# Performance work log

Hardware: AMD Instinct MI355X
Metric: run time of the kernel (lower is better)

## Reference

```python
import jax, jax.numpy as jnp
import numpy as np

TAU = 1.0
TOP_K = 2
TOP_C = 8
EPS = 1e-12


def _stable_softmax(v):
    # matches torch: exp(v - max) / (sum + 1e-12)
    e = jnp.exp(v - jnp.max(v, axis=-1, keepdims=True))
    return e / (jnp.sum(e, axis=-1, keepdims=True) + EPS)


def setup_inputs() -> dict:
    key = jax.random.key(0)
    kx, kw = jax.random.split(key)
    B, D, M = 16384, 2048, 64
    x = jax.random.normal(kx, (B, D), dtype=jnp.float32)
    W = jax.random.normal(kw, (M, D), dtype=jnp.float32) * (1.0 / np.sqrt(D))
    return {"x": x, "W": W}


def reference(x, W):
    # router GEMM: [B, D] x [M, D]^T -> [B, M]
    router_logits = jnp.einsum('bd,md->bm', x, W)
    scaled_logits = router_logits / TAU
    probs = _stable_softmax(scaled_logits)
    # double top-k: first candidates (top_c), then top_k among candidates
    topc_vals, topc_idx = jax.lax.top_k(scaled_logits, TOP_C)   # [B, C]
    topk_vals, topk_pos_in_C = jax.lax.top_k(topc_vals, TOP_K)  # [B, K]
    topk_idx = jnp.take_along_axis(topc_idx, topk_pos_in_C, axis=1)
    topk_weights = _stable_softmax(topk_vals)
    return (topk_idx.astype(jnp.int64), topk_weights, probs, topc_idx.astype(jnp.int64))
```

## Files before the change

### kernel.cpp

```cpp
#include <hip/hip_runtime.h>


typedef __attribute__((ext_vector_type(8))) short short8;
typedef __attribute__((ext_vector_type(4))) float f32x4;

constexpr int Bq = 16384;
constexpr int Dk = 2048;
constexpr int Me = 64;
constexpr int WAVES = 8;
constexpr int ROWS = 32;
constexpr int KCHUNK = Dk / WAVES;
constexpr int NT = KCHUNK / 32;

constexpr size_t OFF_TOPK_IDX = 0;
constexpr size_t OFF_TOPK_W   = (size_t)Bq * 2;
constexpr size_t OFF_PROBS    = (size_t)Bq * 4;
constexpr size_t OFF_TOPC_IDX = (size_t)Bq * 4 + (size_t)Bq * 64;

__device__ __forceinline__ unsigned f2bf2(float lo, float hi) {
  unsigned r;
  asm("v_cvt_pk_bf16_f32 %0, %1, %2" : "=v"(r) : "v"(lo), "v"(hi));
  return r;
}
__device__ __forceinline__ float bflo(unsigned u) { return __builtin_bit_cast(float, u << 16); }
__device__ __forceinline__ float bfhi(unsigned u) { return __builtin_bit_cast(float, u & 0xFFFF0000u); }

__device__ __forceinline__ void split3(const float af[8], short8& s0, short8& s1, short8& s2) {
  uint4 q0, q1, q2;
  unsigned* p0 = &q0.x; unsigned* p1 = &q1.x; unsigned* p2 = &q2.x;
  #pragma unroll
  for (int p = 0; p < 4; ++p) {
    float a = af[2 * p], b = af[2 * p + 1];
    unsigned c0 = f2bf2(a, b);
    float r0a = a - bflo(c0), r0b = b - bfhi(c0);
    unsigned c1 = f2bf2(r0a, r0b);
    float r1a = r0a - bflo(c1), r1b = r0b - bfhi(c1);
    unsigned c2 = f2bf2(r1a, r1b);
    p0[p] = c0; p1[p] = c1; p2[p] = c2;
  }
  s0 = __builtin_bit_cast(short8, q0);
  s1 = __builtin_bit_cast(short8, q1);
  s2 = __builtin_bit_cast(short8, q2);
}

__global__ void wsplit_kernel(const float* __restrict__ W,
                              unsigned short* __restrict__ w0,
                              unsigned short* __restrict__ w1,
                              unsigned short* __restrict__ w2) {
  int t = blockIdx.x * blockDim.x + threadIdx.x;
  int kt = t >> 8, n = (t >> 6) & 3, L = t & 63;
  int e  = n * 16 + (L & 15);
  int kb = kt * 32 + ((L >> 4) << 3);
  const float* src = W + (size_t)e * Dk + kb;
  float4 a = *reinterpret_cast<const float4*>(src);
  float4 b = *reinterpret_cast<const float4*>(src + 4);
  float af[8] = {a.x, a.y, a.z, a.w, b.x, b.y, b.z, b.w};
  short8 s0, s1, s2;
  split3(af, s0, s1, s2);
  *reinterpret_cast<short8*>(w0 + (size_t)t * 8) = s0;
  *reinterpret_cast<short8*>(w1 + (size_t)t * 8) = s1;
  *reinterpret_cast<short8*>(w2 + (size_t)t * 8) = s2;
}

__global__ __launch_bounds__(512, 2)
void gating_mfma(const float* __restrict__ x,
                 const unsigned short* __restrict__ w0,
                 const unsigned short* __restrict__ w1,
                 const unsigned short* __restrict__ w2,
                 float* __restrict__ out) {
  __shared__ __align__(16) char smem[WAVES * ROWS * 36 * 4];
  typedef float XaT[ROWS][36];
  XaT* xa = reinterpret_cast<XaT*>(smem);
  typedef float PartT[ROWS][68];
  PartT* part = reinterpret_cast<PartT*>(smem);

  const int tid  = threadIdx.x;
  const int wv   = tid >> 6;
  const int L    = tid & 63;
  const int lidx = L & 15;
  const int kgrp = L >> 4;
  const int rowBase = blockIdx.x * ROWS;
  const int kBase = wv * KCHUNK;

  const int srow = L >> 3;
  const int sc4  = (L & 7) << 2;
  const float* xg0 = x + (size_t)(rowBase +      srow) * Dk + kBase + sc4;
  const float* xg1 = x + (size_t)(rowBase +  8 + srow) * Dk + kBase + sc4;
  const float* xg2 = x + (size_t)(rowBase + 16 + srow) * Dk + kBase + sc4;
  const float* xg3 = x + (size_t)(rowBase + 24 + srow) * Dk + kBase + sc4;

  const size_t bbase = (size_t)kBase * 64 + (size_t)L * 8;

  f32x4 acc[2][4];
  #pragma unroll
  for (int rg = 0; rg < 2; ++rg)
    #pragma unroll
    for (int n = 0; n < 4; ++n) acc[rg][n] = (f32x4){0.f, 0.f, 0.f, 0.f};

  *reinterpret_cast<float4*>(&xa[wv][     srow][sc4]) = *reinterpret_cast<const float4*>(xg0);
  *reinterpret_cast<float4*>(&xa[wv][ 8 + srow][sc4]) = *reinterpret_cast<const float4*>(xg1);
  *reinterpret_cast<float4*>(&xa[wv][16 + srow][sc4]) = *reinterpret_cast<const float4*>(xg2);
  *reinterpret_cast<float4*>(&xa[wv][24 + srow][sc4]) = *reinterpret_cast<const float4*>(xg3);

  #pragma unroll 1
  for (int kt = 0; kt < NT; ++kt) {
    float4 aLo0 = *reinterpret_cast<const float4*>(&xa[wv][     lidx][kgrp * 8]);
    float4 aHi0 = *reinterpret_cast<const float4*>(&xa[wv][     lidx][kgrp * 8 + 4]);
    float4 aLo1 = *reinterpret_cast<const float4*>(&xa[wv][16 + lidx][kgrp * 8]);
    float4 aHi1 = *reinterpret_cast<const float4*>(&xa[wv][16 + lidx][kgrp * 8 + 4]);

    float4 h0, h1, h2, h3;
    if (kt < NT - 1) {
      h0 = *reinterpret_cast<const float4*>(xg0 + (kt + 1) * 32);
      h1 = *reinterpret_cast<const float4*>(xg1 + (kt + 1) * 32);
      h2 = *reinterpret_cast<const float4*>(xg2 + (kt + 1) * 32);
      h3 = *reinterpret_cast<const float4*>(xg3 + (kt + 1) * 32);
    }

    const size_t to = bbase + (size_t)kt * 2048;

    short8 b0[4];
    #pragma unroll
    for (int n = 0; n < 4; ++n) b0[n] = *reinterpret_cast<const short8*>(w0 + to + n * 512);

    float af0[8] = {aLo0.x, aLo0.y, aLo0.z, aLo0.w, aHi0.x, aHi0.y, aHi0.z, aHi0.w};
    float af1[8] = {aLo1.x, aLo1.y, aLo1.z, aLo1.w, aHi1.x, aHi1.y, aHi1.z, aHi1.w};
    short8 xs00, xs10, xs20, xs01, xs11, xs21;
    split3(af0, xs00, xs10, xs20);
    split3(af1, xs01, xs11, xs21);

    short8 b1[4];
    #pragma unroll
    for (int n = 0; n < 4; ++n) b1[n] = *reinterpret_cast<const short8*>(w1 + to + n * 512);

    #pragma unroll
    for (int n = 0; n < 4; ++n) acc[0][n] = __builtin_amdgcn_mfma_f32_16x16x32_bf16(xs00, b0[n], acc[0][n], 0, 0, 0);
    #pragma unroll
    for (int n = 0; n < 4; ++n) acc[1][n] = __builtin_amdgcn_mfma_f32_16x16x32_bf16(xs01, b0[n], acc[1][n], 0, 0, 0);
    #pragma unroll
    for (int n = 0; n < 4; ++n) acc[0][n] = __builtin_amdgcn_mfma_f32_16x16x32_bf16(xs10, b0[n], acc[0][n], 0, 0, 0);
    #pragma unroll
    for (int n = 0; n < 4; ++n) acc[1][n] = __builtin_amdgcn_mfma_f32_16x16x32_bf16(xs11, b0[n], acc[1][n], 0, 0, 0);
    #pragma unroll
    for (int n = 0; n < 4; ++n) acc[0][n] = __builtin_amdgcn_mfma_f32_16x16x32_bf16(xs20, b0[n], acc[0][n], 0, 0, 0);
    #pragma unroll
    for (int n = 0; n < 4; ++n) acc[1][n] = __builtin_amdgcn_mfma_f32_16x16x32_bf16(xs21, b0[n], acc[1][n], 0, 0, 0);

    short8 b2[4];
    #pragma unroll
    for (int n = 0; n < 4; ++n) b2[n] = *reinterpret_cast<const short8*>(w2 + to + n * 512);

    #pragma unroll
    for (int n = 0; n < 4; ++n) acc[0][n] = __builtin_amdgcn_mfma_f32_16x16x32_bf16(xs00, b1[n], acc[0][n], 0, 0, 0);
    #pragma unroll
    for (int n = 0; n < 4; ++n) acc[1][n] = __builtin_amdgcn_mfma_f32_16x16x32_bf16(xs01, b1[n], acc[1][n], 0, 0, 0);
    #pragma unroll
    for (int n = 0; n < 4; ++n) acc[0][n] = __builtin_amdgcn_mfma_f32_16x16x32_bf16(xs10, b1[n], acc[0][n], 0, 0, 0);
    #pragma unroll
    for (int n = 0; n < 4; ++n) acc[1][n] = __builtin_amdgcn_mfma_f32_16x16x32_bf16(xs11, b1[n], acc[1][n], 0, 0, 0);

    #pragma unroll
    for (int n = 0; n < 4; ++n) acc[0][n] = __builtin_amdgcn_mfma_f32_16x16x32_bf16(xs00, b2[n], acc[0][n], 0, 0, 0);
    #pragma unroll
    for (int n = 0; n < 4; ++n) acc[1][n] = __builtin_amdgcn_mfma_f32_16x16x32_bf16(xs01, b2[n], acc[1][n], 0, 0, 0);

    if (kt < NT - 1) {
      *reinterpret_cast<float4*>(&xa[wv][     srow][sc4]) = h0;
      *reinterpret_cast<float4*>(&xa[wv][ 8 + srow][sc4]) = h1;
      *reinterpret_cast<float4*>(&xa[wv][16 + srow][sc4]) = h2;
      *reinterpret_cast<float4*>(&xa[wv][24 + srow][sc4]) = h3;
    }
  }

  __syncthreads();
  if (wv >= 4) {
    #pragma unroll
    for (int rg = 0; rg < 2; ++rg)
      #pragma unroll
      for (int n = 0; n < 4; ++n)
        #pragma unroll
        for (int r = 0; r < 4; ++r)
          part[wv - 4][rg * 16 + kgrp * 4 + r][n * 16 + lidx] = acc[rg][n][r];
  }
  __syncthreads();
  if (wv < 4) {
    #pragma unroll
    for (int rg = 0; rg < 2; ++rg)
      #pragma unroll
      for (int n = 0; n < 4; ++n)
        #pragma unroll
        for (int r = 0; r < 4; ++r) {
          float s = acc[rg][n][r] + part[wv][rg * 16 + kgrp * 4 + r][n * 16 + lidx];
          part[wv][rg * 16 + kgrp * 4 + r][n * 16 + lidx] = s;
        }
  }
  __syncthreads();

  const int row = tid >> 4;
  const int g   = tid & 15;
  const int c4  = g * 4;
  const size_t grow = (size_t)rowBase + row;

  float4 v = {0.f, 0.f, 0.f, 0.f};
  #pragma unroll
  for (int p = 0; p < 4; ++p) {
    float4 t = *reinterpret_cast<const float4*>(&part[p][row][c4]);
    v.x += t.x; v.y += t.y; v.z += t.z; v.w += t.w;
  }
  float pv[4] = {v.x, v.y, v.z, v.w};

  float mx = fmaxf(fmaxf(pv[0], pv[1]), fmaxf(pv[2], pv[3]));
  #pragma unroll
  for (int m = 1; m < 16; m <<= 1) mx = fmaxf(mx, __shfl_xor(mx, m));
  float e[4], sum = 0.f;
  #pragma unroll
  for (int j = 0; j < 4; ++j) { e[j] = expf(pv[j] - mx); sum += e[j]; }
  #pragma unroll
  for (int m = 1; m < 16; m <<= 1) sum += __shfl_xor(sum, m);
  const float inv = 1.f / (sum + 1e-12f);
  float4 pw = {e[0] * inv, e[1] * inv, e[2] * inv, e[3] * inv};
  *reinterpret_cast<float4*>(out + OFF_PROBS + grow * 64 + c4) = pw;

  unsigned taken = 0;
  int bidx0 = 0, bidx1 = 0;
  float tv0 = 0.f, tv1 = 0.f;
  #pragma unroll 1
  for (int rank = 0; rank < 8; ++rank) {
    float best = -3.4e38f;
    int bl = -1;
    #pragma unroll
    for (int j = 0; j < 4; ++j)
      if (!((taken >> j) & 1u) && pv[j] > best) { best = pv[j]; bl = j; }
    int bidx = (bl >= 0) ? (c4 + bl) : (1 << 30);
    #pragma unroll
    for (int m = 1; m < 16; m <<= 1) {
      float ov = __shfl_xor(best, m);
      int   oi = __shfl_xor(bidx, m);
      if (ov > best || (ov == best && oi < bidx)) { best = ov; bidx = oi; }
    }
    if (bidx >= c4 && bidx < c4 + 4) taken |= 1u << (bidx - c4);
    if (g == 0) out[OFF_TOPC_IDX + grow * 8 + rank] = (float)bidx;
    if (rank == 0) { tv0 = best; bidx0 = bidx; }
    if (rank == 1) { tv1 = best; bidx1 = bidx; }
  }

  if (g == 0) {
    out[OFF_TOPK_IDX + grow * 2 + 0] = (float)bidx0;
    out[OFF_TOPK_IDX + grow * 2 + 1] = (float)bidx1;
    const float e1  = expf(tv1 - tv0);
    const float den = 1.f + e1 + 1e-12f;
    out[OFF_TOPK_W + grow * 2 + 0] = 1.f / den;
    out[OFF_TOPK_W + grow * 2 + 1] = e1 / den;
  }
}

extern "C" void kernel_launch(void* const* d_in, const int* in_sizes, int n_in,
                              void* d_out, int out_size, void* d_ws, size_t ws_size,
                              hipStream_t stream) {
  const float* x = (const float*)d_in[0];
  const float* W = (const float*)d_in[1];
  float* out = (float*)d_out;

  unsigned short* w0 = (unsigned short*)d_ws;
  unsigned short* w1 = w0 + (size_t)Me * Dk;
  unsigned short* w2 = w1 + (size_t)Me * Dk;

  hipLaunchKernelGGL(wsplit_kernel, dim3((Me * Dk / 8) / 256), dim3(256), 0, stream, W, w0, w1, w2);
  hipLaunchKernelGGL(gating_mfma, dim3(Bq / ROWS), dim3(512), 0, stream, x, w0, w1, w2, out);
}
```

Measured before the change: 46.08 us.

## Double row tile to 64 per block to improve weight reuse

Each block now handles 64 rows instead of 32, so every wave loads its W fragments once for four 16-row groups. This halves the weight traffic per row and adds more MFMA work per load. The epilogue is reorganized so 8 threads each cover 8 experts of a row. The cost is more registers and shared memory, launch bounds that drop to one block per SM, and half as many blocks (256), which may leave some of the MI355X's CUs idle.

```diff
diff --git a/kernel.cpp b/kernel.cpp
--- a/kernel.cpp
+++ b/kernel.cpp
@@ -8,9 +8,10 @@
 constexpr int Dk = 2048;
 constexpr int Me = 64;
 constexpr int WAVES = 8;
-constexpr int ROWS = 32;
+constexpr int ROWS = 64;
 constexpr int KCHUNK = Dk / WAVES;
 constexpr int NT = KCHUNK / 32;
+constexpr int XLD = 34;
 
 constexpr size_t OFF_TOPK_IDX = 0;
 constexpr size_t OFF_TOPK_W   = (size_t)Bq * 2;
@@ -62,14 +63,14 @@
   *reinterpret_cast<short8*>(w2 + (size_t)t * 8) = s2;
 }
 
-__global__ __launch_bounds__(512, 2)
+__global__ __launch_bounds__(512, 1)
 void gating_mfma(const float* __restrict__ x,
                  const unsigned short* __restrict__ w0,
                  const unsigned short* __restrict__ w1,
                  const unsigned short* __restrict__ w2,
                  float* __restrict__ out) {
-  __shared__ __align__(16) char smem[WAVES * ROWS * 36 * 4];
-  typedef float XaT[ROWS][36];
+  __shared__ __align__(16) char smem[WAVES * ROWS * XLD * 4];
+  typedef float XaT[ROWS][XLD];
   XaT* xa = reinterpret_cast<XaT*>(smem);
   typedef float PartT[ROWS][68];
   PartT* part = reinterpret_cast<PartT*>(smem);
@@ -84,37 +85,35 @@
 
   const int srow = L >> 3;
   const int sc4  = (L & 7) << 2;
-  const float* xg0 = x + (size_t)(rowBase +      srow) * Dk + kBase + sc4;
-  const float* xg1 = x + (size_t)(rowBase +  8 + srow) * Dk + kBase + sc4;
-  const float* xg2 = x + (size_t)(rowBase + 16 + srow) * Dk + kBase + sc4;
-  const float* xg3 = x + (size_t)(rowBase + 24 + srow) * Dk + kBase + sc4;
+  const float* xgb = x + (size_t)(rowBase + srow) * Dk + kBase + sc4;
 
   const size_t bbase = (size_t)kBase * 64 + (size_t)L * 8;
 
-  f32x4 acc[2][4];
-  #pragma unroll
-  for (int rg = 0; rg < 2; ++rg)
+  f32x4 acc[4][4];
+  #pragma unroll
+  for (int rg = 0; rg < 4; ++rg)
     #pragma unroll
     for (int n = 0; n < 4; ++n) acc[rg][n] = (f32x4){0.f, 0.f, 0.f, 0.f};
 
-  *reinterpret_cast<float4*>(&xa[wv][     srow][sc4]) = *reinterpret_cast<const float4*>(xg0);
-  *reinterpret_cast<float4*>(&xa[wv][ 8 + srow][sc4]) = *reinterpret_cast<const float4*>(xg1);
-  *reinterpret_cast<float4*>(&xa[wv][16 + srow][sc4]) = *reinterpret_cast<const float4*>(xg2);
-  *reinterpret_cast<float4*>(&xa[wv][24 + srow][sc4]) = *reinterpret_cast<const float4*>(xg3);
+  #pragma unroll
+  for (int s = 0; s < 8; ++s)
+    *reinterpret_cast<float4*>(&xa[wv][s * 8 + srow][sc4]) =
+        *reinterpret_cast<const float4*>(xgb + (size_t)s * 8 * Dk);
 
   #pragma unroll 1
   for (int kt = 0; kt < NT; ++kt) {
-    float4 aLo0 = *reinterpret_cast<const float4*>(&xa[wv][     lidx][kgrp * 8]);
-    float4 aHi0 = *reinterpret_cast<const float4*>(&xa[wv][     lidx][kgrp * 8 + 4]);
-    float4 aLo1 = *reinterpret_cast<const float4*>(&xa[wv][16 + lidx][kgrp * 8]);
-    float4 aHi1 = *reinterpret_cast<const float4*>(&xa[wv][16 + lidx][kgrp * 8 + 4]);
-
-    float4 h0, h1, h2, h3;
+    float4 aLo[4], aHi[4];
+    #pragma unroll
+    for (int rg = 0; rg < 4; ++rg) {
+      aLo[rg] = *reinterpret_cast<const float4*>(&xa[wv][rg * 16 + lidx][kgrp * 8]);
+      aHi[rg] = *reinterpret_cast<const float4*>(&xa[wv][rg * 16 + lidx][kgrp * 8 + 4]);
+    }
+
+    float4 h[8];
     if (kt < NT - 1) {
-      h0 = *reinterpret_cast<const float4*>(xg0 + (kt + 1) * 32);
-      h1 = *reinterpret_cast<const float4*>(xg1 + (kt + 1) * 32);
-      h2 = *reinterpret_cast<const float4*>(xg2 + (kt + 1) * 32);
-      h3 = *reinterpret_cast<const float4*>(xg3 + (kt + 1) * 32);
+      #pragma unroll
+      for (int s = 0; s < 8; ++s)
+        h[s] = *reinterpret_cast<const float4*>(xgb + (size_t)s * 8 * Dk + (kt + 1) * 32);
     }
 
     const size_t to = bbase + (size_t)kt * 2048;
@@ -123,59 +122,66 @@
     #pragma unroll
     for (int n = 0; n < 4; ++n) b0[n] = *reinterpret_cast<const short8*>(w0 + to + n * 512);
 
-    float af0[8] = {aLo0.x, aLo0.y, aLo0.z, aLo0.w, aHi0.x, aHi0.y, aHi0.z, aHi0.w};
-    float af1[8] = {aLo1.x, aLo1.y, aLo1.z, aLo1.w, aHi1.x, aHi1.y, aHi1.z, aHi1.w};
-    short8 xs00, xs10, xs20, xs01, xs11, xs21;
-    split3(af0, xs00, xs10, xs20);
-    split3(af1, xs01, xs11, xs21);
+    short8 xs0[4], xs1[4], xs2[4];
+    #pragma unroll
+    for (int rg = 0; rg < 4; ++rg) {
+      float af[8] = {aLo[rg].x, aLo[rg].y, aLo[rg].z, aLo[rg].w,
+                     aHi[rg].x, aHi[rg].y, aHi[rg].z, aHi[rg].w};
+      split3(af, xs0[rg], xs1[rg], xs2[rg]);
+    }
 
     short8 b1[4];
     #pragma unroll
     for (int n = 0; n < 4; ++n) b1[n] = *reinterpret_cast<const short8*>(w1 + to + n * 512);
 
     #pragma unroll
-    for (int n = 0; n < 4; ++n) acc[0][n] = __builtin_amdgcn_mfma_f32_16x16x32_bf16(xs00, b0[n], acc[0][n], 0, 0, 0);
-    #pragma unroll
-    for (int n = 0; n < 4; ++n) acc[1][n] = __builtin_amdgcn_mfma_f32_16x16x32_bf16(xs01, b0[n], acc[1][n], 0, 0, 0);
-    #pragma unroll
-    for (int n = 0; n < 4; ++n) acc[0][n] = __builtin_amdgcn_mfma_f32_16x16x32_bf16(xs10, b0[n], acc[0][n], 0, 0, 0);
-    #pragma unroll
-    for (int n = 0; n < 4; ++n) acc[1][n] = __builtin_amdgcn_mfma_f32_16x16x32_bf16(xs11, b0[n], acc[1][n], 0, 0, 0);
-    #pragma unroll
-    for (int n = 0; n < 4; ++n) acc[0][n] = __builtin_amdgcn_mfma_f32_16x16x32_bf16(xs20, b0[n], acc[0][n], 0, 0, 0);
-    #pragma unroll
-    for (int n = 0; n < 4; ++n) acc[1][n] = __builtin_amdgcn_mfma_f32_16x16x32_bf16(xs21, b0[n], acc[1][n], 0, 0, 0);
+    for (int rg = 0; rg < 4; ++rg)
+      #pragma unroll
+      for (int n = 0; n < 4; ++n)
+        acc[rg][n] = __builtin_amdgcn_mfma_f32_16x16x32_bf16(xs0[rg], b0[n], acc[rg][n], 0, 0, 0);
+    #pragma unroll
+    for (int rg = 0; rg < 4; ++rg)
+      #pragma unroll
+      for (int n = 0; n < 4; ++n)
+        acc[rg][n] = __builtin_amdgcn_mfma_f32_16x16x32_bf16(xs1[rg], b0[n], acc[rg][n], 0, 0, 0);
+    #pragma unroll
+    for (int rg = 0; rg < 4; ++rg)
+      #pragma unroll
+      for (int n = 0; n < 4; ++n)
+        acc[rg][n] = __builtin_amdgcn_mfma_f32_16x16x32_bf16(xs2[rg], b0[n], acc[rg][n], 0, 0, 0);
 
     short8 b2[4];
     #pragma unroll
     for (int n = 0; n < 4; ++n) b2[n] = *reinterpret_cast<const short8*>(w2 + to + n * 512);
 
     #pragma unroll
-    for (int n = 0; n < 4; ++n) acc[0][n] = __builtin_amdgcn_mfma_f32_16x16x32_bf16(xs00, b1[n], acc[0][n], 0, 0, 0);
-    #pragma unroll
-    for (int n = 0; n < 4; ++n) acc[1][n] = __builtin_amdgcn_mfma_f32_16x16x32_bf16(xs01, b1[n], acc[1][n], 0, 0, 0);
-    #pragma unroll
-    for (int n = 0; n < 4; ++n) acc[0][n] = __builtin_amdgcn_mfma_f32_16x16x32_bf16(xs10, b1[n], acc[0][n], 0, 0, 0);
-    #pragma unroll
-    for (int n = 0; n < 4; ++n) acc[1][n] = __builtin_amdgcn_mfma_f32_16x16x32_bf16(xs11, b1[n], acc[1][n], 0, 0, 0);
-
-    #pragma unroll
-    for (int n = 0; n < 4; ++n) acc[0][n] = __builtin_amdgcn_mfma_f32_16x16x32_bf16(xs00, b2[n], acc[0][n], 0, 0, 0);
-    #pragma unroll
-    for (int n = 0; n < 4; ++n) acc[1][n] = __builtin_amdgcn_mfma_f32_16x16x32_bf16(xs01, b2[n], acc[1][n], 0, 0, 0);
+    for (int rg = 0; rg < 4; ++rg)
+      #pragma unroll
+      for (int n = 0; n < 4; ++n)
+        acc[rg][n] = __builtin_amdgcn_mfma_f32_16x16x32_bf16(xs0[rg], b1[n], acc[rg][n], 0, 0, 0);
+    #pragma unroll
+    for (int rg = 0; rg < 4; ++rg)
+      #pragma unroll
+      for (int n = 0; n < 4; ++n)
+        acc[rg][n] = __builtin_amdgcn_mfma_f32_16x16x32_bf16(xs1[rg], b1[n], acc[rg][n], 0, 0, 0);
+
+    #pragma unroll
+    for (int rg = 0; rg < 4; ++rg)
+      #pragma unroll
+      for (int n = 0; n < 4; ++n)
+        acc[rg][n] = __builtin_amdgcn_mfma_f32_16x16x32_bf16(xs0[rg], b2[n], acc[rg][n], 0, 0, 0);
 
     if (kt < NT - 1) {
-      *reinterpret_cast<float4*>(&xa[wv][     srow][sc4]) = h0;
-      *reinterpret_cast<float4*>(&xa[wv][ 8 + srow][sc4]) = h1;
-      *reinterpret_cast<float4*>(&xa[wv][16 + srow][sc4]) = h2;
-      *reinterpret_cast<float4*>(&xa[wv][24 + srow][sc4]) = h3;
+      #pragma unroll
+      for (int s = 0; s < 8; ++s)
+        *reinterpret_cast<float4*>(&xa[wv][s * 8 + srow][sc4]) = h[s];
     }
   }
 
   __syncthreads();
   if (wv >= 4) {
     #pragma unroll
-    for (int rg = 0; rg < 2; ++rg)
+    for (int rg = 0; rg < 4; ++rg)
       #pragma unroll
       for (int n = 0; n < 4; ++n)
         #pragma unroll
@@ -185,7 +191,7 @@
   __syncthreads();
   if (wv < 4) {
     #pragma unroll
-    for (int rg = 0; rg < 2; ++rg)
+    for (int rg = 0; rg < 4; ++rg)
       #pragma unroll
       for (int n = 0; n < 4; ++n)
         #pragma unroll
@@ -196,30 +202,40 @@
   }
   __syncthreads();
 
-  const int row = tid >> 4;
-  const int g   = tid & 15;
-  const int c4  = g * 4;
+  const int row = tid >> 3;
+  const int g   = tid & 7;
+  const int c8  = g * 8;
   const size_t grow = (size_t)rowBase + row;
 
-  float4 v = {0.f, 0.f, 0.f, 0.f};
-  #pragma unroll
-  for (int p = 0; p < 4; ++p) {
-    float4 t = *reinterpret_cast<const float4*>(&part[p][row][c4]);
-    v.x += t.x; v.y += t.y; v.z += t.z; v.w += t.w;
-  }
-  float pv[4] = {v.x, v.y, v.z, v.w};
-
-  float mx = fmaxf(fmaxf(pv[0], pv[1]), fmaxf(pv[2], pv[3]));
-  #pragma unroll
-  for (int m = 1; m < 16; m <<= 1) mx = fmaxf(mx, __shfl_xor(mx, m));
-  float e[4], sum = 0.f;
-  #pragma unroll
-  for (int j = 0; j < 4; ++j) { e[j] = expf(pv[j] - mx); sum += e[j]; }
-  #pragma unroll
-  for (int m = 1; m < 16; m <<= 1) sum += __shfl_xor(sum, m);
+  float pv[8];
+  {
+    float4 va = {0.f, 0.f, 0.f, 0.f}, vb = {0.f, 0.f, 0.f, 0.f};
+    #pragma unroll
+    for (int p = 0; p < 4; ++p) {
+      float4 ta = *reinterpret_cast<const float4*>(&part[p][row][c8]);
+      float4 tb = *reinterpret_cast<const float4*>(&part[p][row][c8 + 4]);
+      va.x += ta.x; va.y += ta.y; va.z += ta.z; va.w += ta.w;
+      vb.x += tb.x; vb.y += tb.y; vb.z += tb.z; vb.w += tb.w;
+    }
+    pv[0] = va.x; pv[1] = va.y; pv[2] = va.z; pv[3] = va.w;
+    pv[4] = vb.x; pv[5] = vb.y; pv[6] = vb.z; pv[7] = vb.w;
+  }
+
+  float mx = pv[0];
+  #pragma unroll
+  for (int j = 1; j < 8; ++j) mx = fmaxf(mx, pv[j]);
+  #pragma unroll
+  for (int m = 1; m < 8; m <<= 1) mx = fmaxf(mx, __shfl_xor(mx, m));
+  float e[8], sum = 0.f;
+  #pragma unroll
+  for (int j = 0; j < 8; ++j) { e[j] = expf(pv[j] - mx); sum += e[j]; }
+  #pragma unroll
+  for (int m = 1; m < 8; m <<= 1) sum += __shfl_xor(sum, m);
   const float inv = 1.f / (sum + 1e-12f);
-  float4 pw = {e[0] * inv, e[1] * inv, e[2] * inv, e[3] * inv};
-  *reinterpret_cast<float4*>(out + OFF_PROBS + grow * 64 + c4) = pw;
+  float4 pwa = {e[0] * inv, e[1] * inv, e[2] * inv, e[3] * inv};
+  float4 pwb = {e[4] * inv, e[5] * inv, e[6] * inv, e[7] * inv};
+  *reinterpret_cast<float4*>(out + OFF_PROBS + grow * 64 + c8) = pwa;
+  *reinterpret_cast<float4*>(out + OFF_PROBS + grow * 64 + c8 + 4) = pwb;
 
   unsigned taken = 0;
   int bidx0 = 0, bidx1 = 0;
@@ -229,16 +245,16 @@
     float best = -3.4e38f;
     int bl = -1;
     #pragma unroll
-    for (int j = 0; j < 4; ++j)
+    for (int j = 0; j < 8; ++j)
       if (!((taken >> j) & 1u) && pv[j] > best) { best = pv[j]; bl = j; }
-    int bidx = (bl >= 0) ? (c4 + bl) : (1 << 30);
-    #pragma unroll
-    for (int m = 1; m < 16; m <<= 1) {
+    int bidx = (bl >= 0) ? (c8 + bl) : (1 << 30);
+    #pragma unroll
+    for (int m = 1; m < 8; m <<= 1) {
       float ov = __shfl_xor(best, m);
       int   oi = __shfl_xor(bidx, m);
       if (ov > best || (ov == best && oi < bidx)) { best = ov; bidx = oi; }
     }
-    if (bidx >= c4 && bidx < c4 + 4) taken |= 1u << (bidx - c4);
+    if (bidx >= c8 && bidx < c8 + 8) taken |= 1u << (bidx - c8);
     if (g == 0) out[OFF_TOPC_IDX + grow * 8 + rank] = (float)bidx;
     if (rank == 0) { tv0 = best; bidx0 = bidx; }
     if (rank == 1) { tv1 = best; bidx1 = bidx; }
```

Measured after the change: 70.24 us. 1.52x slower.
